# Kernel optimization log

Hardware: AMD Instinct MI355X
Metric: run time of the kernel (lower is better)

The kernel has to match this reference:

```python
import jax, jax.numpy as jnp
import numpy as np

H = 256; DS = 8; DC = 4; DI = 512; DTR = 16; NH = 4; EPS = 1e-5
B, N, F, E, S, LC = 8, 512, 32, 8192, 512, 8


def setup_inputs() -> dict:
    key = jax.random.key(0)
    ks = iter(jax.random.split(key, 64))
    def rn(shape, s=0.05):
        return jax.random.normal(next(ks), shape, jnp.float32) * s
    z = lambda *s: jnp.zeros(s, jnp.float32)
    inp = dict(
        node_features=jax.random.normal(next(ks), (B, N, F), jnp.float32),
        edge_index=jax.random.randint(next(ks), (B, 2, E), 0, N),
        W_init=rn((F, H)), b_init=z(H),
        gcn1_W=rn((H, H)), gcn1_b=z(H),
        gcn2_W=rn((H, H)), gcn2_b=z(H),
        in_proj_W=rn((H, 2 * DI)),
        conv_W=rn((DI, DC)), conv_b=z(DI),
        xproj_W=rn((DI, DTR + 2 * DS)),
        dt_W=rn((DTR, DI)), dt_b=z(DI),
        A_log=jnp.log(jnp.tile(jnp.arange(1, DS + 1, dtype=jnp.float32), (DI, 1))),
        Dp=jnp.ones((DI,), jnp.float32),
        out_W=rn((DI, H)),
        Wq=rn((H, H)), bq=z(H), Wk=rn((H, H)), bk=z(H), Wv=rn((H, H)), bv=z(H),
        Wo=rn((H, H)), bo=z(H),
        fus_W=rn((3 * H, H)), fus_b=z(H),
        ln_g=jnp.ones((H,), jnp.float32), ln_b=z(H),
        cw=rn((H, 1)), cb=z(1), hw=rn((H, 4)), hb=z(4), tw=rn((H, 3)), tb=z(3),
        p1w=rn((H, S)), p1b=z(S), p2w=rn((H, S)), p2b=z(S),
        dw=rn((H, S)), db=z(S), sw=rn((H, LC)), sb=z(LC))
    return inp


def gcn(x, src, dst, W, b):
    # PyG GCNConv: self-loops + symmetric deg^{-1/2} normalization, scatter-add.
    n = x.shape[0]
    loops = jnp.arange(n)
    s = jnp.concatenate([src, loops]); d = jnp.concatenate([dst, loops])
    deg = jax.ops.segment_sum(jnp.ones_like(d, x.dtype), d, n)
    dinv = jnp.where(deg > 0, jax.lax.rsqrt(deg), 0.0)
    norm = (dinv[s] * dinv[d])[:, None]
    m = x @ W
    return jax.ops.segment_sum(m[s] * norm, d, n) + b


def mamba(x, in_W, conv_W, conv_b, xproj_W, dt_W, dt_b, A_log, Dp, out_W):
    # mamba_ssm Mamba block, batch=1, seq len L = total nodes.
    L = x.shape[0]
    xz = x @ in_W
    xc, zg = xz[:, :DI], xz[:, DI:]
    xp = jnp.pad(xc, ((DC - 1, 0), (0, 0)))            # causal depthwise conv
    win = xp[jnp.arange(L)[:, None] + jnp.arange(DC)[None, :]]  # [L,K,DI]
    xc = jax.nn.silu(jnp.einsum('lkd,dk->ld', win, conv_W) + conv_b)
    proj = xc @ xproj_W
    dt, Bm, Cm = proj[:, :DTR], proj[:, DTR:DTR + DS], proj[:, DTR + DS:]
    delta = jax.nn.softplus(dt @ dt_W + dt_b)           # [L,DI]
    A = -jnp.exp(A_log)                                 # [DI,DS]
    dA = jnp.exp(delta[:, :, None] * A[None])           # [L,DI,DS]
    dBx = delta[:, :, None] * Bm[:, None, :] * xc[:, :, None]
    def step(h, inp):
        dA_t, dBx_t, C_t = inp
        h = dA_t * h + dBx_t
        return h, (h * C_t[None, :]).sum(-1)
    _, y = jax.lax.scan(step, jnp.zeros((DI, DS), x.dtype), (dA, dBx, Cm))
    y = (y + Dp * xc) * jax.nn.silu(zg)
    return y @ out_W


def mha(x, Wq, bq, Wk, bk, Wv, bv, Wo, bo):
    L = x.shape[0]; hd = H // NH
    q = (x @ Wq + bq).reshape(L, NH, hd)
    k = (x @ Wk + bk).reshape(L, NH, hd)
    v = (x @ Wv + bv).reshape(L, NH, hd)
    s = jnp.einsum('qhd,khd->hqk', q, k) / np.float32(np.sqrt(hd))
    a = jax.nn.softmax(s, axis=-1)
    o = jnp.einsum('hqk,khd->qhd', a, v).reshape(L, H)
    return o @ Wo + bo


def _forward(node_features, edge_index, W_init, b_init, gcn1_W, gcn1_b, gcn2_W, gcn2_b,
             in_proj_W, conv_W, conv_b, xproj_W, dt_W, dt_b, A_log, Dp, out_W,
             Wq, bq, Wk, bk, Wv, bv, Wo, bo, fus_W, fus_b, ln_g, ln_b,
             cw, cb, hw, hb, tw, tb, p1w, p1b, p2w, p2b, dw, db, sw, sb):
    Bsz, Nn, Ff = node_features.shape
    x = node_features.reshape(Bsz * Nn, Ff)
    # offset per-graph edge indices into the flat node space (batching loop)
    ei = (edge_index + (jnp.arange(Bsz) * Nn)[:, None, None]).transpose(1, 0, 2).reshape(2, -1)
    src, dst = ei[0], ei[1]
    h = jax.nn.relu(x @ W_init + b_init)
    h = jax.nn.relu(gcn(h, src, dst, gcn1_W, gcn1_b))
    h = jax.nn.relu(gcn(h, src, dst, gcn2_W, gcn2_b))
    m = mamba(h, in_proj_W, conv_W, conv_b, xproj_W, dt_W, dt_b, A_log, Dp, out_W)
    a = mha(h, Wq, bq, Wk, bk, Wv, bv, Wo, bo)
    fused = jax.nn.relu(jnp.concatenate([h, m, a], -1) @ fus_W + fus_b)
    res = fused + h
    mu = res.mean(-1, keepdims=True)
    var = ((res - mu) ** 2).mean(-1, keepdims=True)
    hf = (res - mu) * jax.lax.rsqrt(var + EPS) * ln_g + ln_b
    batch = jnp.repeat(jnp.arange(Bsz), Nn)
    pooled = jax.ops.segment_sum(hf, batch, Bsz) / jnp.float32(Nn)  # global_mean_pool
    outs = [pooled @ cw + cb, pooled @ hw + hb, pooled @ tw + tb,
            pooled @ p1w + p1b, pooled @ p2w + p2b, pooled @ dw + db,
            pooled @ sw + sb]
    return jnp.concatenate(outs, -1)  # [B, 1+4+3+S+S+S+LC]


def reference(node_features, edge_index, W_init, b_init, gcn1_W, gcn1_b, gcn2_W, gcn2_b,
              in_proj_W, conv_W, conv_b, xproj_W, dt_W, dt_b, A_log, Dp, out_W,
              Wq, bq, Wk, bk, Wv, bv, Wo, bo, fus_W, fus_b, ln_g, ln_b,
              cw, cb, hw, hb, tw, tb, p1w, p1b, p2w, p2b, dw, db, sw, sb):
    return _forward(node_features, edge_index, W_init, b_init, gcn1_W, gcn1_b, gcn2_W, gcn2_b,
                    in_proj_W, conv_W, conv_b, xproj_W, dt_W, dt_b, A_log, Dp, out_W,
                    Wq, bq, Wk, bk, Wv, bv, Wo, bo, fus_W, fus_b, ln_g, ln_b,
                    cw, cb, hw, hb, tw, tb, p1w, p1b, p2w, p2b, dw, db, sw, sb)
```

## Files before the change

kernel.cpp:

```cpp
#include <hip/hip_runtime.h>
#include <hip/hip_bf16.h>
#include <math.h>

typedef __hip_bfloat16 hbf;
typedef short bf16x8 __attribute__((ext_vector_type(8)));
typedef float f32x4 __attribute__((ext_vector_type(4)));

constexpr int NL  = 4096;
constexpr int HH  = 256;
constexpr int NE  = 8192;
constexpr int DIc = 512;
constexpr int DSc = 8;
constexpr int CLc = 16;
constexpr int NOUT = 12416;

constexpr size_t O_MBUF  = 0;
constexpr size_t O_QK    = 1048576;
constexpr size_t O_H2    = 2097152;
constexpr size_t O_CATB  = 3145728;
constexpr size_t O_XZB   = 4718592;
constexpr size_t O_XC    = 6815744;
constexpr size_t O_DELTA = 8912896;
constexpr size_t O_PROJ  = 11010048;
constexpr size_t O_HST   = 11141120;
constexpr size_t O_Y     = 12189696;
constexpr size_t O_POOL  = 13238272;
constexpr size_t O_DINV  = 13240320;
constexpr size_t O_B768  = 13244416;
constexpr size_t O_INT   = 13245184;
constexpr size_t O_WT    = 13327112;
constexpr size_t O_XB    = 13839112;
constexpr size_t O_H0B   = 13904648;
constexpr size_t O_H2B   = 14428936;
constexpr size_t O_XCB   = 14953224;
constexpr size_t O_DTAB  = 16001800;
constexpr size_t O_QKB   = 16067584;
constexpr size_t O_VTB   = 17116160;
constexpr size_t O_PART  = 17640448;
constexpr size_t O_HWT   = 17902592;

constexpr int NW = 12;
__device__ __constant__ int wc_cum[NW+1] = {
    0, 8192, 73728, 139264, 155648, 172032, 303104, 565248,
    630784, 696320, 761856, 827392, 1024000 };
__device__ __constant__ int wc_K [NW] = {32,256,256,512,16,512,256,256,256,256,256,768};
__device__ __constant__ int wc_N [NW] = {256,256,256,32,512,256,1024,256,256,256,256,256};
__device__ __constant__ int wc_Kp[NW] = {32,256,256,512,32,512,256,256,256,256,256,768};
struct WSrc { const float* p[NW]; };
struct HSrc { const float* p[7]; };
struct OPtrs { hbf* p[8]; };

__device__ __constant__ int hw_b[8]  = {0,1,5,8,520,1032,1544,1552};
__device__ __constant__ int hw_nc[7] = {1,4,3,512,512,512,8};

constexpr int PR_W = 1024000;
constexpr int PR_X = PR_W + 131072;
constexpr int PR_B = PR_X + 768;
constexpr int PR_P = PR_B + 262144;
constexpr int PR_I = PR_P + 4096;
constexpr int PR_H = PR_I + 397312;
__global__ __launch_bounds__(256) void prep_k(WSrc ws, hbf* __restrict__ wt,
        const float* __restrict__ x, hbf* __restrict__ xb,
        const float* __restrict__ bq, const float* __restrict__ bk,
        const float* __restrict__ bv,
        float* __restrict__ b768, float* __restrict__ part, int* __restrict__ cnt,
        HSrc hs, hbf* __restrict__ hwt) {
    int idx = blockIdx.x*256 + threadIdx.x;
    if (idx < PR_W) {
        int lo = 0, hi = NW-1;
        while (lo < hi) { int mid = (lo+hi+1)>>1; if (idx >= wc_cum[mid]) lo = mid; else hi = mid-1; }
        int local = idx - wc_cum[lo];
        int Kp = wc_Kp[lo], K = wc_K[lo], N = wc_N[lo];
        int n = local / Kp, k = local - n*Kp;
        float v = (k < K) ? ws.p[lo][(size_t)k*N + n] : 0.0f;
        wt[idx] = __float2bfloat16(v);
    } else if (idx < PR_X) {
        int i = idx - PR_W;
        xb[i] = __float2bfloat16(x[i]);
    } else if (idx < PR_B) {
        int i = idx - PR_X;
        b768[i] = (i < 256) ? bq[i] : (i < 512 ? bk[i-256] : bv[i-512]);
    } else if (idx < PR_P) {
        part[idx - PR_B] = 0.0f;
    } else if (idx < PR_I) {
        cnt[idx - PR_P] = 0;
    } else if (idx < PR_H) {
        int i = idx - PR_I;
        int j = i >> 8, k = i & 255;
        int seg = 0;
        while (j >= hw_b[seg+1]) seg++;
        int col = j - hw_b[seg], nc = hw_nc[seg];
        hwt[(size_t)j*256 + k] = __float2bfloat16(hs.p[seg][(size_t)k*nc + col]);
    }
}

__global__ void bucket_k(const int* __restrict__ ei, int* __restrict__ cnt,
                         int* __restrict__ csr) {
    int i = blockIdx.x*256 + threadIdx.x;
    int b = i >> 13, e = i & 8191;
    int src = ei[b*2*NE + e]      + (b << 9);
    int dst = ei[b*2*NE + NE + e] + (b << 9);
    int slot = atomicAdd(&cnt[dst], 1);
    if (slot < 64) csr[(dst << 6) + slot] = src;
}

__global__ __launch_bounds__(256) void gather_k(const hbf* __restrict__ m,
                        const int* __restrict__ csr, const int* __restrict__ cnt,
                        hbf* __restrict__ outb) {
    int n = blockIdx.x, c = threadIdx.x;
    int cn = min(cnt[n], 64);
    float dn = rsqrtf(1.0f + (float)cn);
    float acc = __bfloat162float(m[(size_t)n*HH + c]) * dn * dn;
    for (int e = 0; e < cn; e++) {
        int s = csr[(n << 6) + e];
        float ds = rsqrtf(1.0f + (float)min(cnt[s], 64));
        acc += __bfloat162float(m[(size_t)s*HH + c]) * (ds * dn);
    }
    outb[(size_t)n*HH + c] = __float2bfloat16(acc);
}

template<int ACT, int OUTM>
__global__ __launch_bounds__(256) void mg_k(const unsigned short* __restrict__ A,
        const unsigned short* __restrict__ Bt, const float* __restrict__ bias,
        void* __restrict__ Cp, int ldc, void* __restrict__ Cp2, void* __restrict__ Cp3,
        const float* __restrict__ resid, int ldr, int M, int K, int N)
{
    __shared__ __align__(16) unsigned short Asm[2][32][40];
    __shared__ __align__(16) unsigned short Bsm[2][32][40];
    int t = threadIdx.x;
    int lane = t & 63, w = t >> 6;
    int wr = (w & 1) * 16, wc = (w >> 1) * 16;
    int row0 = blockIdx.x * 32, col0 = blockIdx.y * 32;
    int sr = t >> 3, sk8 = (t & 7) * 8;
    f32x4 acc = {};
    int fr = lane & 15, fq8 = (lane >> 4) * 8;

    uint4 zz = make_uint4(0u,0u,0u,0u);
    uint4 ra = zz, rb = zz;
    if (sk8 < K) {
        ra = *(const uint4*)&A[(size_t)(row0+sr)*K + sk8];
        rb = *(const uint4*)&Bt[(size_t)(col0+sr)*K + sk8];
    }

    for (int k0 = 0; k0 < K; k0 += 64) {
        __syncthreads();
        *(uint4*)&Asm[sk8>>5][sr][sk8 & 31] = ra;
        *(uint4*)&Bsm[sk8>>5][sr][sk8 & 31] = rb;
        __syncthreads();
        int kn = k0 + 64;
        if (kn < K) {
            ra = rb = zz;
            if (kn + sk8 < K) {
                ra = *(const uint4*)&A[(size_t)(row0+sr)*K + kn + sk8];
                rb = *(const uint4*)&Bt[(size_t)(col0+sr)*K + kn + sk8];
            }
        }
        #pragma unroll
        for (int ks = 0; ks < 2; ks++) {
            bf16x8 a = *(bf16x8*)&Asm[ks][wr + fr][fq8];
            bf16x8 b = *(bf16x8*)&Bsm[ks][wc + fr][fq8];
            acc = __builtin_amdgcn_mfma_f32_16x16x32_bf16(a, b, acc, 0, 0, 0);
        }
    }

    int fc = lane & 15, frq = (lane >> 4) * 4;
    if constexpr (OUTM == 4) {
        int col = wc + fc;
        #pragma unroll
        for (int i = 0; i < 4; i++) {
            int row = row0 + wr + frq + i;
            float v = acc[i];
            ((float*)Cp)[(size_t)row*32 + col] = v;
            ((hbf*)Cp2)[(size_t)row*32 + col] = __float2bfloat16((col < 16) ? v : 0.0f);
        }
    } else if constexpr (OUTM == 5) {
        if (col0 < 1024) {
            int col = col0 + wc + fc;
            #pragma unroll
            for (int i = 0; i < 4; i++) {
                int row = row0 + wr + frq + i;
                ((hbf*)Cp)[(size_t)row*1024 + col] = __float2bfloat16(acc[i]);
            }
        } else if (col0 < 1536) {
            int gcol = col0 + wc + fc;
            int col = gcol - 1024;
            float bvv = bias[col];
            float sc = (col < 256) ? 0.125f : 1.0f;
            #pragma unroll
            for (int i = 0; i < 4; i++) {
                int row = row0 + wr + frq + i;
                ((hbf*)Cp2)[(size_t)row*512 + col] = __float2bfloat16((acc[i] + bvv) * sc);
            }
        } else {
            __shared__ __align__(16) unsigned short Ts[32][48];
            int gcol = col0 + wc + fc;
            float bvv = bias[gcol - 1024];
            #pragma unroll
            for (int i = 0; i < 4; i++)
                *(hbf*)&Ts[wc + fc][wr + frq + i] = __float2bfloat16(acc[i] + bvv);
            __syncthreads();
            if (t < 128) {
                int c = t >> 2, rs = (t & 3) * 8;
                *(uint4*)((hbf*)Cp3 + (size_t)(col0 - 1536 + c)*NL + row0 + rs) = *(uint4*)&Ts[c][rs];
            }
        }
    } else if constexpr (OUTM == 6) {
        int col = col0 + wc + fc;
        float bvv = bias[col];
        #pragma unroll
        for (int i = 0; i < 4; i++) {
            int row = row0 + wr + frq + i;
            float v = fmaxf(acc[i] + bvv, 0.0f);
            ((float*)Cp)[(size_t)row*HH + col] = v;
            hbf hv = __float2bfloat16(v);
            ((hbf*)Cp2)[(size_t)row*HH + col] = hv;
            ((hbf*)Cp3)[(size_t)row*768 + col] = hv;
        }
    } else {
        int col = col0 + wc + fc;
        if (col < N) {
            float bvv = bias ? bias[col] : 0.0f;
            #pragma unroll
            for (int i = 0; i < 4; i++) {
                int row = row0 + wr + frq + i;
                float v = acc[i] + bvv;
                if (ACT == 1) v = fmaxf(v, 0.0f);
                if (ACT == 2) v = (v > 20.0f) ? v : log1pf(expf(v));
                if (resid) v += resid[(size_t)row*ldr + col];
                if (OUTM == 0) ((float*)Cp)[(size_t)row*ldc + col] = v;
                else           ((hbf*)Cp)[(size_t)row*ldc + col] = __float2bfloat16(v);
            }
        }
    }
}

__global__ __launch_bounds__(256) void conv_k(const hbf* __restrict__ xzb,
                       const float* __restrict__ cW,
                       const float* __restrict__ cb, hbf* __restrict__ xcb) {
    int i = blockIdx.x*256 + threadIdx.x;
    int l = i >> 6, d8 = (i & 63) << 3;
    float acc[8];
    {
        float4 c0 = *(const float4*)&cb[d8];
        float4 c1 = *(const float4*)&cb[d8+4];
        acc[0]=c0.x; acc[1]=c0.y; acc[2]=c0.z; acc[3]=c0.w;
        acc[4]=c1.x; acc[5]=c1.y; acc[6]=c1.z; acc[7]=c1.w;
    }
    float4 cw4[8];
    #pragma unroll
    for (int j = 0; j < 8; j++) cw4[j] = *(const float4*)&cW[(d8+j)*4];
    #pragma unroll
    for (int k = 0; k < 4; k++) {
        int ls = l - 3 + k;
        if (ls < 0) continue;
        bf16x8 v = *(const bf16x8*)&xzb[(size_t)ls*1024 + d8];
        #pragma unroll
        for (int j = 0; j < 8; j++) {
            short tv = v[j]; hbf hv; *(short*)&hv = tv;
            float wk = (k == 0) ? cw4[j].x : (k == 1) ? cw4[j].y : (k == 2) ? cw4[j].z : cw4[j].w;
            acc[j] += __bfloat162float(hv) * wk;
        }
    }
    hbf out[8];
    #pragma unroll
    for (int j = 0; j < 8; j++) {
        float r = acc[j] / (1.0f + __expf(-acc[j]));
        out[j] = __float2bfloat16(r);
    }
    *(uint4*)&xcb[(size_t)l*512 + d8] = *(uint4*)out;
}

__global__ __launch_bounds__(256) void scan1_k(const float* __restrict__ delta,
                        const hbf* __restrict__ xc, const float* __restrict__ proj,
                        const float* __restrict__ Alog,
                        float* __restrict__ P, float* __restrict__ Hl)
{
    int c = blockIdx.x >> 1;
    int d = ((blockIdx.x & 1) << 8) + threadIdx.x;
    float Ac[DSc], pr[DSc], h[DSc];
    #pragma unroll
    for (int s2 = 0; s2 < DSc; s2++) { Ac[s2] = -__expf(Alog[d*DSc+s2]); pr[s2]=1.0f; h[s2]=0.0f; }
    int l0 = c * CLc;
    for (int l = l0; l < l0 + CLc; l++) {
        float dl = delta[(size_t)l*DIc + d];
        float dx = dl * __bfloat162float(xc[(size_t)l*DIc + d]);
        const float* pb = proj + l*32 + 16;
        #pragma unroll
        for (int s2 = 0; s2 < DSc; s2++) {
            float a = __expf(dl * Ac[s2]);
            h[s2] = a*h[s2] + dx*pb[s2];
            pr[s2] *= a;
        }
    }
    #pragma unroll
    for (int s2 = 0; s2 < DSc; s2++) {
        P [(size_t)(c*DSc+s2)*DIc + d] = pr[s2];
        Hl[(size_t)(c*DSc+s2)*DIc + d] = h[s2];
    }
}

__global__ __launch_bounds__(256) void scan2t_k(const float* __restrict__ P,
                        const float* __restrict__ Hl, float* __restrict__ Hst) {
    __shared__ float Ps[256][17], Hs[256][17];
    int t = threadIdx.x, sg = blockIdx.x;
    int si = t & 15, cb = t >> 4;
    #pragma unroll
    for (int it = 0; it < 16; it++) {
        int c = it*16 + cb;
        size_t off = (size_t)c*4096 + sg*16 + si;
        Ps[c][si] = P[off];
        Hs[c][si] = Hl[off];
    }
    __syncthreads();
    int si2 = t >> 4, g = t & 15;
    int lane = t & 63;
    float Pg = 1.0f, Hg = 0.0f;
    #pragma unroll
    for (int j = 0; j < 16; j++) {
        int c = g*16 + j;
        float pc = Ps[c][si2], hc = Hs[c][si2];
        Hg = hc + pc*Hg;
        Pg = pc*Pg;
    }
    #pragma unroll
    for (int off = 1; off < 16; off <<= 1) {
        float Pp = __shfl(Pg, lane - off);
        float Hp = __shfl(Hg, lane - off);
        if (g >= off) { Hg = Hg + Pg*Hp; Pg = Pg*Pp; }
    }
    float carry = __shfl(Hg, lane - 1);
    if (g == 0) carry = 0.0f;
    float h = carry;
    #pragma unroll
    for (int j = 0; j < 16; j++) {
        int c = g*16 + j;
        float pc = Ps[c][si2], hc = Hs[c][si2];
        Hs[c][si2] = h;
        h = hc + pc*h;
    }
    __syncthreads();
    #pragma unroll
    for (int it = 0; it < 16; it++) {
        int c = it*16 + cb;
        Hst[(size_t)c*4096 + sg*16 + si] = Hs[c][si];
    }
}

__global__ __launch_bounds__(256) void scan3_k(const float* __restrict__ delta,
                        const hbf* __restrict__ xc, const float* __restrict__ proj,
                        const float* __restrict__ Alog, const float* __restrict__ Hst,
                        const float* __restrict__ Dp, const hbf* __restrict__ xzb,
                        hbf* __restrict__ Y)
{
    int c = blockIdx.x >> 1;
    int d = ((blockIdx.x & 1) << 8) + threadIdx.x;
    float Ac[DSc], h[DSc];
    #pragma unroll
    for (int s2 = 0; s2 < DSc; s2++) {
        Ac[s2] = -__expf(Alog[d*DSc+s2]);
        h[s2]  = Hst[(size_t)(c*DSc+s2)*DIc + d];
    }
    float dpv = Dp[d];
    int l0 = c * CLc;
    for (int l = l0; l < l0 + CLc; l++) {
        float dl = delta[(size_t)l*DIc + d];
        float xv = __bfloat162float(xc[(size_t)l*DIc + d]);
        float dx = dl * xv;
        const float* pb = proj + l*32 + 16;
        float y = 0.0f;
        #pragma unroll
        for (int s2 = 0; s2 < DSc; s2++) {
            float a = __expf(dl * Ac[s2]);
            h[s2] = a*h[s2] + dx*pb[s2];
            y += h[s2] * pb[8+s2];
        }
        float z = __bfloat162float(xzb[(size_t)l*1024 + 512 + d]);
        float sz = z / (1.0f + __expf(-z));
        Y[(size_t)l*DIc + d] = __float2bfloat16((y + dpv*xv) * sz);
    }
}

__global__ __launch_bounds__(512, 8) void attn_part_k(const unsigned short* __restrict__ QK,
                       const unsigned short* __restrict__ Vt,
                       OPtrs op, float* __restrict__ lsum)
{
    __shared__ __align__(16) unsigned short QPs[128][72];
    __shared__ __align__(16) unsigned short Ks[64][72];
    __shared__ __align__(16) unsigned short Vs[64][72];
    int t = threadIdx.x, lane = t & 63, w = t >> 6;
    int h = blockIdx.y, q0 = blockIdx.x * 128, skc = blockIdx.z;
    int fm = lane & 15, fq = lane >> 4;

    {
        int qr = t >> 2, qc = (t & 3) * 16;
        const unsigned short* src = &QK[(size_t)(q0+qr)*512 + h*64 + qc];
        *(uint4*)&QPs[qr][qc]     = *(const uint4*)&src[0];
        *(uint4*)&QPs[qr][qc + 8] = *(const uint4*)&src[8];
    }
    __syncthreads();
    bf16x8 qa[2];
    #pragma unroll
    for (int ks = 0; ks < 2; ks++)
        qa[ks] = *(bf16x8*)&QPs[w*16 + fm][ks*32 + fq*8];

    bf16x8 ones;
    #pragma unroll
    for (int j = 0; j < 8; j++) ones[j] = (short)0x3F80;

    f32x4 o[4] = {};
    f32x4 ol = {};
    int sr = t >> 3, sk = (t & 7) * 8;
    const unsigned short* Kb = QK + 256;
    int kt = skc * 512;
    uint4 ka = *(const uint4*)&Kb[(size_t)(kt+sr)*512 + h*64 + sk];
    uint4 va = *(const uint4*)&Vt[(size_t)(h*64+sr)*NL + kt + sk];

    for (int it = 0; it < 8; it++) {
        __syncthreads();
        *(uint4*)&Ks[sr][sk] = ka;
        *(uint4*)&Vs[sr][sk] = va;
        __syncthreads();
        if (it < 7) {
            int kn = kt + 64;
            ka = *(const uint4*)&Kb[(size_t)(kn+sr)*512 + h*64 + sk];
            va = *(const uint4*)&Vt[(size_t)(h*64+sr)*NL + kn + sk];
        }
        #pragma unroll
        for (int np = 0; np < 2; np++) {
            f32x4 s0 = {}, s1 = {};
            __builtin_amdgcn_s_setprio(1);
            #pragma unroll
            for (int ks = 0; ks < 2; ks++) {
                bf16x8 kb0 = *(bf16x8*)&Ks[(np*2+0)*16 + fm][ks*32 + fq*8];
                bf16x8 kb1 = *(bf16x8*)&Ks[(np*2+1)*16 + fm][ks*32 + fq*8];
                s0 = __builtin_amdgcn_mfma_f32_16x16x32_bf16(qa[ks], kb0, s0, 0, 0, 0);
                s1 = __builtin_amdgcn_mfma_f32_16x16x32_bf16(qa[ks], kb1, s1, 0, 0, 0);
            }
            __builtin_amdgcn_s_setprio(0);
            #pragma unroll
            for (int i = 0; i < 4; i++) {
                float p0 = __expf(s0[i] - 4.0f);
                float p1 = __expf(s1[i] - 4.0f);
                *(hbf*)&QPs[w*16 + fq*4 + i][(np*2+0)*16 + fm] = __float2bfloat16(p0);
                *(hbf*)&QPs[w*16 + fq*4 + i][(np*2+1)*16 + fm] = __float2bfloat16(p1);
            }
        }
        __builtin_amdgcn_s_setprio(1);
        #pragma unroll
        for (int ks = 0; ks < 2; ks++) {
            bf16x8 pa = *(bf16x8*)&QPs[w*16 + fm][ks*32 + fq*8];
            #pragma unroll
            for (int nt = 0; nt < 4; nt++) {
                bf16x8 vb = *(bf16x8*)&Vs[nt*16 + fm][ks*32 + fq*8];
                o[nt] = __builtin_amdgcn_mfma_f32_16x16x32_bf16(pa, vb, o[nt], 0, 0, 0);
            }
            ol = __builtin_amdgcn_mfma_f32_16x16x32_bf16(pa, ones, ol, 0, 0, 0);
        }
        __builtin_amdgcn_s_setprio(0);
        kt += 64;
    }
    hbf* Op = op.p[skc];
    #pragma unroll
    for (int i = 0; i < 4; i++) {
        int row = w*16 + fq*4 + i;
        #pragma unroll
        for (int nt = 0; nt < 4; nt++)
            Op[(size_t)(q0 + row)*HH + h*64 + nt*16 + fm] = __float2bfloat16(o[nt][i]);
    }
    if (fm == 0) {
        #pragma unroll
        for (int i = 0; i < 4; i++)
            lsum[(size_t)(skc*4 + h)*NL + q0 + w*16 + fq*4 + i] = ol[i];
    }
}

__global__ __launch_bounds__(256) void amerge_k(OPtrs op, const float* __restrict__ lsum,
                                                hbf* __restrict__ aob) {
    int t = threadIdx.x;
    int row = blockIdx.x*8 + (t >> 5);
    int d8 = (t & 31) << 3;
    int h = d8 >> 6;
    float L = 0.0f;
    #pragma unroll
    for (int c = 0; c < 8; c++) L += lsum[(size_t)(c*4 + h)*NL + row];
    float inv = 1.0f / L;
    float s[8] = {};
    #pragma unroll
    for (int c = 0; c < 8; c++) {
        bf16x8 v = *(const bf16x8*)&op.p[c][(size_t)row*HH + d8];
        #pragma unroll
        for (int j = 0; j < 8; j++) {
            short tv = v[j]; hbf hv; *(short*)&hv = tv;
            s[j] += __bfloat162float(hv);
        }
    }
    hbf out[8];
    #pragma unroll
    for (int j = 0; j < 8; j++) out[j] = __float2bfloat16(s[j] * inv);
    *(uint4*)&aob[(size_t)row*HH + d8] = *(uint4*)out;
}

__global__ __launch_bounds__(256) void ln_k(const float* __restrict__ X,
                    const float* __restrict__ g, const float* __restrict__ b,
                    float* __restrict__ part) {
    __shared__ float red[4];
    int r = blockIdx.x, t = threadIdx.x;
    float v = X[(size_t)r*HH + t];
    float s = v;
    #pragma unroll
    for (int o = 32; o > 0; o >>= 1) s += __shfl_down(s, o);
    if ((t & 63) == 0) red[t >> 6] = s;
    __syncthreads();
    float mean = (red[0]+red[1]+red[2]+red[3]) * (1.0f/256.0f);
    float dfv = v - mean;
    float s2 = dfv*dfv;
    #pragma unroll
    for (int o = 32; o > 0; o >>= 1) s2 += __shfl_down(s2, o);
    __syncthreads();
    if ((t & 63) == 0) red[t >> 6] = s2;
    __syncthreads();
    float var = (red[0]+red[1]+red[2]+red[3]) * (1.0f/256.0f);
    float y = dfv * rsqrtf(var + 1e-5f) * g[t] + b[t];
    atomicAdd(&part[(size_t)(r & 127)*2048 + (r >> 9)*HH + t], y * (1.0f/512.0f));
}

__global__ void reduce_k(const float* __restrict__ part, float* __restrict__ pooled) {
    int i = blockIdx.x*256 + threadIdx.x;
    float s = 0.0f;
    #pragma unroll 8
    for (int p = 0; p < 128; p++) s += part[(size_t)p*2048 + i];
    pooled[i] = s;
}

__global__ __launch_bounds__(256) void heads_k(const float* __restrict__ pooled,
        const hbf* __restrict__ hwt,
        const float* cbh, const float* hb, const float* tb, const float* p1b,
        const float* p2b, const float* db, const float* sb, float* __restrict__ out)
{
    int idx = blockIdx.x*4 + (threadIdx.x >> 6);
    int lane = threadIdx.x & 63;
    if (idx >= NOUT) return;
    int b = idx / 1552, j = idx - b*1552;
    const float* bi; int col;
    if (j < 1)         { bi = cbh; col = j;        }
    else if (j < 5)    { bi = hb;  col = j - 1;    }
    else if (j < 8)    { bi = tb;  col = j - 5;    }
    else if (j < 520)  { bi = p1b; col = j - 8;    }
    else if (j < 1032) { bi = p2b; col = j - 520;  }
    else if (j < 1544) { bi = db;  col = j - 1032; }
    else               { bi = sb;  col = j - 1544; }
    const float* pl = pooled + b*HH;
    const hbf* wr = hwt + (size_t)j*256;
    int k4 = lane * 4;
    float4 pv = *(const float4*)&pl[k4];
    short4 wv = *(const short4*)&wr[k4];
    hbf w0, w1, w2, w3;
    *(short*)&w0 = wv.x; *(short*)&w1 = wv.y; *(short*)&w2 = wv.z; *(short*)&w3 = wv.w;
    float s = pv.x*__bfloat162float(w0) + pv.y*__bfloat162float(w1)
            + pv.z*__bfloat162float(w2) + pv.w*__bfloat162float(w3);
    #pragma unroll
    for (int o = 32; o > 0; o >>= 1) s += __shfl_down(s, o);
    if (lane == 0) out[idx] = s + bi[col];
}

extern "C" void kernel_launch(void* const* d_in, const int* in_sizes, int n_in,
                              void* d_out, int out_size, void* d_ws, size_t ws_size,
                              hipStream_t stream)
{
    (void)in_sizes; (void)n_in; (void)out_size; (void)ws_size;
    const float* x      = (const float*)d_in[0];
    const int*   ei     = (const int*)  d_in[1];
    const float* W_init = (const float*)d_in[2];
    const float* b_init = (const float*)d_in[3];
    const float* g1W = (const float*)d_in[4];
    const float* g1b = (const float*)d_in[5];
    const float* g2W = (const float*)d_in[6];
    const float* g2b = (const float*)d_in[7];
    const float* inW = (const float*)d_in[8];
    const float* cW  = (const float*)d_in[9];
    const float* cb  = (const float*)d_in[10];
    const float* xpW = (const float*)d_in[11];
    const float* dtW = (const float*)d_in[12];
    const float* dtb = (const float*)d_in[13];
    const float* Alog= (const float*)d_in[14];
    const float* Dp  = (const float*)d_in[15];
    const float* outW= (const float*)d_in[16];
    const float* Wq  = (const float*)d_in[17];
    const float* bq  = (const float*)d_in[18];
    const float* Wk  = (const float*)d_in[19];
    const float* bk  = (const float*)d_in[20];
    const float* Wv  = (const float*)d_in[21];
    const float* bv  = (const float*)d_in[22];
    const float* Wo  = (const float*)d_in[23];
    const float* bo  = (const float*)d_in[24];
    const float* fusW= (const float*)d_in[25];
    const float* fusb= (const float*)d_in[26];
    const float* lng = (const float*)d_in[27];
    const float* lnb = (const float*)d_in[28];
    const float* cwp = (const float*)d_in[29];
    const float* cbp = (const float*)d_in[30];
    const float* hwp = (const float*)d_in[31];
    const float* hbp = (const float*)d_in[32];
    const float* twp = (const float*)d_in[33];
    const float* tbp = (const float*)d_in[34];
    const float* p1w = (const float*)d_in[35];
    const float* p1b = (const float*)d_in[36];
    const float* p2w = (const float*)d_in[37];
    const float* p2b = (const float*)d_in[38];
    const float* dwp = (const float*)d_in[39];
    const float* dbp = (const float*)d_in[40];
    const float* swp = (const float*)d_in[41];
    const float* sbp = (const float*)d_in[42];

    float* fw = (float*)d_ws;
    int* iw = (int*)(fw + O_INT);
    int* cnt = iw;
    int* csr = (int*)(fw + O_XC);

    hbf* wt   = (hbf*)(fw + O_WT);
    hbf* xb   = (hbf*)(fw + O_XB);
    hbf* h0b  = (hbf*)(fw + O_H0B);
    hbf* h2b  = (hbf*)(fw + O_H2B);
    hbf* xcb  = (hbf*)(fw + O_XCB);
    hbf* dtab = (hbf*)(fw + O_DTAB);
    hbf* xzb  = (hbf*)(fw + O_XZB);
    hbf* yb   = (hbf*)(fw + O_Y);
    hbf* aob  = (hbf*)(fw + O_Y);
    hbf* catb = (hbf*)(fw + O_CATB);
    hbf* qkB  = (hbf*)(fw + O_QKB);
    hbf* vtB  = (hbf*)(fw + O_VTB);
    hbf* aggb = (hbf*)(fw + O_MBUF);
    float* fused = fw + O_XC;
    float* b768 = fw + O_B768;
    float* part = fw + O_PART;
    hbf* hwt  = (hbf*)(fw + O_HWT);

    float* scanP  = fw + O_MBUF;
    float* scanHl = fw + O_QK;
    float* scanHst= fw + O_HST;
    float* lsum   = fw + O_HST;

    OPtrs op;
    op.p[0] = (hbf*)(fw + O_MBUF);
    op.p[1] = (hbf*)(fw + O_MBUF + 524288);
    op.p[2] = (hbf*)(fw + O_DELTA);
    op.p[3] = (hbf*)(fw + O_DELTA + 524288);
    op.p[4] = (hbf*)(fw + O_DELTA + 1048576);
    op.p[5] = (hbf*)(fw + O_DELTA + 1572864);
    op.p[6] = (hbf*)(fw + O_XZB);
    op.p[7] = (hbf*)(fw + O_XZB + 524288);

    hbf* WtInit  = wt + 0;
    hbf* WtG1    = wt + 8192;
    hbf* WtG2    = wt + 73728;
    hbf* WtXp    = wt + 139264;
    hbf* WtDt    = wt + 155648;
    hbf* WtOut   = wt + 172032;
    hbf* WtInQKV = wt + 303104;
    hbf* WtO     = wt + 761856;
    hbf* WtFus   = wt + 827392;

    WSrc wsrc;
    wsrc.p[0]=W_init; wsrc.p[1]=g1W; wsrc.p[2]=g2W; wsrc.p[3]=xpW; wsrc.p[4]=dtW;
    wsrc.p[5]=outW; wsrc.p[6]=inW; wsrc.p[7]=Wq; wsrc.p[8]=Wk; wsrc.p[9]=Wv;
    wsrc.p[10]=Wo; wsrc.p[11]=fusW;
    HSrc hsrc;
    hsrc.p[0]=cwp; hsrc.p[1]=hwp; hsrc.p[2]=twp; hsrc.p[3]=p1w;
    hsrc.p[4]=p2w; hsrc.p[5]=dwp; hsrc.p[6]=swp;
    prep_k<<<(PR_H+255)/256,256,0,stream>>>(wsrc, wt, x, xb, bq, bk, bv, b768,
                                            part, cnt, hsrc, hwt);

    bucket_k<<<256,256,0,stream>>>(ei, cnt, csr);

    mg_k<1,1><<<dim3(128,8),256,0,stream>>>((const unsigned short*)xb, (const unsigned short*)WtInit,
        b_init, h0b, 256, nullptr, nullptr, nullptr, 0, NL, 32, 256);
    gather_k<<<4096,256,0,stream>>>(h0b, csr, cnt, aggb);
    mg_k<1,1><<<dim3(128,8),256,0,stream>>>((const unsigned short*)aggb, (const unsigned short*)WtG1,
        g1b, h0b, 256, nullptr, nullptr, nullptr, 0, NL, 256, 256);
    gather_k<<<4096,256,0,stream>>>(h0b, csr, cnt, aggb);
    mg_k<1,6><<<dim3(128,8),256,0,stream>>>((const unsigned short*)aggb, (const unsigned short*)WtG2,
        g2b, fw+O_H2, 256, h2b, catb, nullptr, 0, NL, 256, 256);

    mg_k<0,5><<<dim3(128,56),256,0,stream>>>((const unsigned short*)h2b, (const unsigned short*)WtInQKV,
        b768, xzb, 1024, qkB, vtB, nullptr, 0, NL, 256, 1792);

    conv_k<<<1024,256,0,stream>>>(xzb, cW, cb, xcb);
    mg_k<0,4><<<dim3(128,1),256,0,stream>>>((const unsigned short*)xcb, (const unsigned short*)WtXp,
        nullptr, fw+O_PROJ, 32, dtab, nullptr, nullptr, 0, NL, 512, 32);
    mg_k<2,0><<<dim3(128,16),256,0,stream>>>((const unsigned short*)dtab, (const unsigned short*)WtDt,
        dtb, fw+O_DELTA, 512, nullptr, nullptr, nullptr, 0, NL, 32, 512);
    scan1_k<<<512,256,0,stream>>>(fw+O_DELTA, xcb, fw+O_PROJ, Alog, scanP, scanHl);
    scan2t_k<<<256,256,0,stream>>>(scanP, scanHl, scanHst);
    scan3_k<<<512,256,0,stream>>>(fw+O_DELTA, xcb, fw+O_PROJ, Alog, scanHst, Dp, xzb, yb);
    mg_k<0,1><<<dim3(128,8),256,0,stream>>>((const unsigned short*)yb, (const unsigned short*)WtOut,
        nullptr, catb + 256, 768, nullptr, nullptr, nullptr, 0, NL, 512, 256);

    attn_part_k<<<dim3(32,4,8),512,0,stream>>>((const unsigned short*)qkB,
        (const unsigned short*)vtB, op, lsum);
    amerge_k<<<512,256,0,stream>>>(op, lsum, aob);
    mg_k<0,1><<<dim3(128,8),256,0,stream>>>((const unsigned short*)aob, (const unsigned short*)WtO,
        bo, catb + 512, 768, nullptr, nullptr, nullptr, 0, NL, 256, 256);

    mg_k<1,0><<<dim3(128,8),256,0,stream>>>((const unsigned short*)catb, (const unsigned short*)WtFus,
        fusb, fused, 256, nullptr, nullptr, fw+O_H2, 256, NL, 768, 256);
    ln_k<<<4096,256,0,stream>>>(fused, lng, lnb, part);
    reduce_k<<<8,256,0,stream>>>(part, fw+O_POOL);
    heads_k<<<(NOUT+3)/4,256,0,stream>>>(fw+O_POOL, hwt, cbp,hbp,tbp,p1b,p2b,dbp,sbp,
                                         (float*)d_out);
}
```

Baseline: 342.0 us.

## Keep attention probabilities in registers via transposed MFMA, skip LDS round-trip

The QK^T product is now computed transposed (K as A operand), so each lane's accumulator holds the layout the PV MFMA needs as its B operand. Probabilities are packed directly into a bf16x4 register and fed to 16x16x16 MFMAs instead of being written to and reread from shared memory. This removes LDS stores and loads of P per tile. The cost is more, smaller MFMA instructions, and outputs are stored transposed with packed 8-byte writes.

```diff
diff --git a/kernel.cpp b/kernel.cpp
--- a/kernel.cpp
+++ b/kernel.cpp
@@ -4,6 +4,7 @@
 
 typedef __hip_bfloat16 hbf;
 typedef short bf16x8 __attribute__((ext_vector_type(8)));
+typedef short bf16x4 __attribute__((ext_vector_type(4)));
 typedef float f32x4 __attribute__((ext_vector_type(4)));
 
 constexpr int NL  = 4096;
@@ -403,9 +404,9 @@
     for (int ks = 0; ks < 2; ks++)
         qa[ks] = *(bf16x8*)&QPs[w*16 + fm][ks*32 + fq*8];
 
-    bf16x8 ones;
-    #pragma unroll
-    for (int j = 0; j < 8; j++) ones[j] = (short)0x3F80;
+    bf16x4 ones4;
+    #pragma unroll
+    for (int j = 0; j < 4; j++) ones4[j] = (short)0x3F80;
 
     f32x4 o[4] = {};
     f32x4 ol = {};
@@ -426,52 +427,43 @@
             va = *(const uint4*)&Vt[(size_t)(h*64+sr)*NL + kn + sk];
         }
         #pragma unroll
-        for (int np = 0; np < 2; np++) {
-            f32x4 s0 = {}, s1 = {};
+        for (int nt = 0; nt < 4; nt++) {
+            f32x4 s = {};
             __builtin_amdgcn_s_setprio(1);
             #pragma unroll
             for (int ks = 0; ks < 2; ks++) {
-                bf16x8 kb0 = *(bf16x8*)&Ks[(np*2+0)*16 + fm][ks*32 + fq*8];
-                bf16x8 kb1 = *(bf16x8*)&Ks[(np*2+1)*16 + fm][ks*32 + fq*8];
-                s0 = __builtin_amdgcn_mfma_f32_16x16x32_bf16(qa[ks], kb0, s0, 0, 0, 0);
-                s1 = __builtin_amdgcn_mfma_f32_16x16x32_bf16(qa[ks], kb1, s1, 0, 0, 0);
+                bf16x8 kb = *(bf16x8*)&Ks[nt*16 + fm][ks*32 + fq*8];
+                s = __builtin_amdgcn_mfma_f32_16x16x32_bf16(kb, qa[ks], s, 0, 0, 0);
             }
             __builtin_amdgcn_s_setprio(0);
+            bf16x4 pb;
             #pragma unroll
             for (int i = 0; i < 4; i++) {
-                float p0 = __expf(s0[i] - 4.0f);
-                float p1 = __expf(s1[i] - 4.0f);
-                *(hbf*)&QPs[w*16 + fq*4 + i][(np*2+0)*16 + fm] = __float2bfloat16(p0);
-                *(hbf*)&QPs[w*16 + fq*4 + i][(np*2+1)*16 + fm] = __float2bfloat16(p1);
+                hbf ph = __float2bfloat16(__expf(s[i] - 4.0f));
+                pb[i] = *(short*)&ph;
             }
-        }
-        __builtin_amdgcn_s_setprio(1);
-        #pragma unroll
-        for (int ks = 0; ks < 2; ks++) {
-            bf16x8 pa = *(bf16x8*)&QPs[w*16 + fm][ks*32 + fq*8];
+            __builtin_amdgcn_s_setprio(1);
             #pragma unroll
-            for (int nt = 0; nt < 4; nt++) {
-                bf16x8 vb = *(bf16x8*)&Vs[nt*16 + fm][ks*32 + fq*8];
-                o[nt] = __builtin_amdgcn_mfma_f32_16x16x32_bf16(pa, vb, o[nt], 0, 0, 0);
+            for (int ntd = 0; ntd < 4; ntd++) {
+                bf16x4 va4 = *(bf16x4*)&Vs[ntd*16 + fm][nt*16 + fq*4];
+                o[ntd] = __builtin_amdgcn_mfma_f32_16x16x16bf16_1k(va4, pb, o[ntd], 0, 0, 0);
             }
-            ol = __builtin_amdgcn_mfma_f32_16x16x32_bf16(pa, ones, ol, 0, 0, 0);
-        }
-        __builtin_amdgcn_s_setprio(0);
+            ol = __builtin_amdgcn_mfma_f32_16x16x16bf16_1k(ones4, pb, ol, 0, 0, 0);
+            __builtin_amdgcn_s_setprio(0);
+        }
         kt += 64;
     }
     hbf* Op = op.p[skc];
-    #pragma unroll
-    for (int i = 0; i < 4; i++) {
-        int row = w*16 + fq*4 + i;
-        #pragma unroll
-        for (int nt = 0; nt < 4; nt++)
-            Op[(size_t)(q0 + row)*HH + h*64 + nt*16 + fm] = __float2bfloat16(o[nt][i]);
-    }
-    if (fm == 0) {
-        #pragma unroll
-        for (int i = 0; i < 4; i++)
-            lsum[(size_t)(skc*4 + h)*NL + q0 + w*16 + fq*4 + i] = ol[i];
-    }
+    int orow = q0 + w*16 + fm;
+    #pragma unroll
+    for (int ntd = 0; ntd < 4; ntd++) {
+        hbf ov[4] __attribute__((aligned(8)));
+        #pragma unroll
+        for (int i = 0; i < 4; i++) ov[i] = __float2bfloat16(o[ntd][i]);
+        *(uint2*)&Op[(size_t)orow*HH + h*64 + ntd*16 + fq*4] = *(uint2*)ov;
+    }
+    if (fq == 0)
+        lsum[(size_t)(skc*4 + h)*NL + q0 + w*16 + fm] = ol[0];
 }
 
 __global__ __launch_bounds__(256) void amerge_k(OPtrs op, const float* __restrict__ lsum,
```

New measurement: 337.7 us. Within noise of the previous version (-1.3%).
